# Performance work log

Hardware: AMD Instinct MI355X
Metric: run time of the kernel (lower is better)

Reference implementation:

```python
import jax, jax.numpy as jnp
import numpy as np

B, S = 2, 2048
HQ, HKV, D = 32, 8, 128
SCALING = 0.08838834764831845  # 1/sqrt(128)
E4M3_MAX = 448.0
FP4_MAX = 6.0
# e2m1 representable magnitudes and decision midpoints
FP4_GRID = jnp.array([0.0, 0.5, 1.0, 1.5, 2.0, 3.0, 4.0, 6.0], dtype=jnp.float32)
FP4_MID = (FP4_GRID[:-1] + FP4_GRID[1:]) / 2.0


def quant_dequant_e4m3(x):
    """Simulate torch .to(float8_e4m3fn): clamp to +-448, round mantissa to 3 bits."""
    ax = jnp.abs(x)
    xc = jnp.clip(x, -E4M3_MAX, E4M3_MAX)
    e = jnp.clip(jnp.floor(jnp.log2(jnp.maximum(ax, 1e-12))), -6.0, 8.0)
    q = jnp.round(xc * jnp.exp2(3.0 - e)) * jnp.exp2(e - 3.0)
    return jnp.where(ax == 0.0, 0.0, q)


def quant_dequant_fp4(x):
    """FP4 (e2m1) compress/decompress with per-(token,head) absmax scale over head_dim.
    x: [B, S, H, D] -> dequantized [B, S, H, D]."""
    scale = jnp.max(jnp.abs(x), axis=-1, keepdims=True) / FP4_MAX  # [B,S,H,1]
    scale = jnp.maximum(scale, 1e-12)
    xn = x / scale
    idx = jnp.searchsorted(FP4_MID, jnp.abs(xn))  # nearest e2m1 magnitude
    return jnp.sign(xn) * FP4_GRID[idx] * scale


def setup_inputs() -> dict:
    key = jax.random.key(0)
    kq, kk, kv = jax.random.split(key, 3)
    q = jax.random.normal(kq, (B, S, HQ * D), dtype=jnp.float32)
    k = jax.random.normal(kk, (B, S, HKV * D), dtype=jnp.float32)
    v = jax.random.normal(kv, (B, S, HKV * D), dtype=jnp.float32)
    return {"q": q, "k": k, "v": v}


def reference(q, k, v):
    # reshape to heads
    qh = q.reshape(B, S, HQ, D)
    kh = k.reshape(B, S, HKV, D)
    vh = v.reshape(B, S, HKV, D)
    # FP8 cast then FP4 compress/decompress of the KV cache
    kq8 = quant_dequant_e4m3(kh)
    vq8 = quant_dequant_e4m3(vh)
    kd = quant_dequant_fp4(kq8)
    vd = quant_dequant_fp4(vq8)
    # GQA: expand kv heads to query heads
    g = HQ // HKV
    kr = jnp.repeat(kd, g, axis=2)  # [B,S,HQ,D]
    vr = jnp.repeat(vd, g, axis=2)
    scores = jnp.einsum("bqhd,bkhd->bhqk", qh, kr) * SCALING  # [B,HQ,S,S]
    causal = jnp.tril(jnp.ones((S, S), dtype=bool))
    scores = jnp.where(causal[None, None], scores, jnp.float32(-1e30))
    probs = jax.nn.softmax(scores, axis=-1)
    out = jnp.einsum("bhqk,bkhd->bqhd", probs, vr)
    return out.reshape(B, S, HQ * D)
```

## Files before the change

### kernel.cpp

```cpp
#include <hip/hip_runtime.h>
#include <cstdint>
#include <cstddef>

#define B_    2
#define S_    2048
#define HQ_   32
#define HKV_  8
#define D_    128
#define QSCALE_ (0.08838834764831845f * 1.4426950408889634f)

#define NROW_ (B_*S_*HKV_)

typedef __bf16 bf16x8 __attribute__((ext_vector_type(8)));
typedef float  f32x4  __attribute__((ext_vector_type(4)));
typedef unsigned int u32x4 __attribute__((ext_vector_type(4)));

__device__ __forceinline__ unsigned int f2bfu(float f) {
    __bf16 b = (__bf16)f;
    return (unsigned int)__builtin_bit_cast(unsigned short, b);
}

__device__ __forceinline__ void gl_lds16(const unsigned short* g, unsigned short* l) {
    __builtin_amdgcn_global_load_lds(
        (const __attribute__((address_space(1))) void*)g,
        (__attribute__((address_space(3))) void*)l, 16, 0, 0);
}

__device__ __forceinline__ float qd_e4m3(float x) {
    float ax = fabsf(x);
    float xc = fminf(fmaxf(x, -448.f), 448.f);
    float axc = fmaxf(ax, 1e-12f);
    int e = (int)((__builtin_bit_cast(unsigned int, axc) >> 23) & 255u) - 127;
    e = min(max(e, -6), 8);
    float s1 = __builtin_bit_cast(float, (unsigned int)(130 - e) << 23);
    float s2 = __builtin_bit_cast(float, (unsigned int)(124 + e) << 23);
    float q = rintf(xc * s1) * s2;
    return ax == 0.f ? 0.f : q;
}

__device__ __forceinline__ float qd_fp4(float x, float scale) {
    float xn = x / scale;
    float a = fabsf(xn);
    float g;
    if      (a <= 0.25f) g = 0.f;
    else if (a <= 0.75f) g = 0.5f;
    else if (a <= 1.25f) g = 1.f;
    else if (a <= 1.75f) g = 1.5f;
    else if (a <= 2.5f)  g = 2.f;
    else if (a <= 3.5f)  g = 3.f;
    else if (a <= 5.f)   g = 4.f;
    else                 g = 6.f;
    return copysignf(g * scale, xn);
}

__global__ __launch_bounds__(256) void prep(const float* __restrict__ k,
                                            const float* __restrict__ v,
                                            unsigned short* __restrict__ kd,
                                            unsigned short* __restrict__ vdT) {
    __shared__ alignas(16) unsigned short t[64][136];
    if (blockIdx.x < 8192) {
        int gw = (blockIdx.x * 256 + threadIdx.x) >> 6;
        int lane = threadIdx.x & 63;
        int row = gw;
        int b   = row / (S_ * HKV_);
        int rem = row - b * (S_ * HKV_);
        int s   = rem >> 3;
        int h   = rem & 7;
        float2 x = *(const float2*)(k + (size_t)row * D_ + 2 * lane);
        float q0 = qd_e4m3(x.x);
        float q1 = qd_e4m3(x.y);
        float amax = fmaxf(fabsf(q0), fabsf(q1));
#pragma unroll
        for (int m = 1; m < 64; m <<= 1) amax = fmaxf(amax, __shfl_xor(amax, m, 64));
        float scale = fmaxf(amax / 6.0f, 1e-12f);
        float y0 = qd_fp4(q0, scale);
        float y1 = qd_fp4(q1, scale);
        size_t outOff = ((size_t)(b * HKV_ + h) * S_ + s) * D_ + 2 * lane;
        unsigned int pack = f2bfu(y0) | (f2bfu(y1) << 16);
        *(unsigned int*)(kd + outOff) = pack;
    } else {
        int bid = blockIdx.x - 8192;
        int bh = bid >> 5;
        int st = bid & 31;
        int s0 = st * 64;
        int b = bh >> 3;
        int h = bh & 7;
        int tid = threadIdx.x;
        int lane = tid & 63;
        int wave = tid >> 6;
#pragma unroll
        for (int i = 0; i < 8; ++i) {
            int rA = wave * 16 + 2 * i;
            const float* srcA = v + (((size_t)b * S_ + (s0 + rA)) * HKV_ + h) * D_ + 2 * lane;
            const float* srcB = srcA + (size_t)HKV_ * D_;
            float2 xA = *(const float2*)srcA;
            float2 xB = *(const float2*)srcB;
            float a0 = qd_e4m3(xA.x), a1 = qd_e4m3(xA.y);
            float c0 = qd_e4m3(xB.x), c1 = qd_e4m3(xB.y);
            float amA = fmaxf(fabsf(a0), fabsf(a1));
            float amB = fmaxf(fabsf(c0), fabsf(c1));
#pragma unroll
            for (int m = 1; m < 64; m <<= 1) {
                amA = fmaxf(amA, __shfl_xor(amA, m, 64));
                amB = fmaxf(amB, __shfl_xor(amB, m, 64));
            }
            float sA = fmaxf(amA / 6.0f, 1e-12f);
            float sB = fmaxf(amB / 6.0f, 1e-12f);
            unsigned int pA = f2bfu(qd_fp4(a0, sA)) | (f2bfu(qd_fp4(a1, sA)) << 16);
            unsigned int pB = f2bfu(qd_fp4(c0, sB)) | (f2bfu(qd_fp4(c1, sB)) << 16);
            *(unsigned int*)&t[rA][2 * lane]     = pA;
            *(unsigned int*)&t[rA + 1][2 * lane] = pB;
        }
        __syncthreads();
        int d = tid >> 1;
        unsigned short* dp = vdT + ((size_t)bh * D_ + d) * S_ + s0;
#pragma unroll
        for (int i = 0; i < 4; ++i) {
            int c = (tid & 1) + 2 * i;
            int so = c * 8;
            unsigned short tmp[8];
#pragma unroll
            for (int e = 0; e < 8; ++e) tmp[e] = t[so + e][d];
            *(uint4*)(dp + so) = *(uint4*)tmp;
        }
    }
}

__global__ __launch_bounds__(256) void attn(const float* __restrict__ q,
                                            const unsigned short* __restrict__ kd,
                                            const unsigned short* __restrict__ vdT,
                                            float* __restrict__ out) {
    int bh = blockIdx.x;
    int qt = 31 - blockIdx.y;
    int b  = bh >> 5;
    int hq = bh & 31;
    int hkv = hq >> 2;
    int tid  = threadIdx.x;
    int lane = tid & 63;
    int wave = tid >> 6;
    int m16  = lane & 15;
    int g    = lane >> 4;
    int m8   = m16 & 7;

    __shared__ alignas(16) unsigned short ks[64 * 128];
    __shared__ alignas(16) unsigned short vs[128 * 64];

    const unsigned short* kbase = kd  + (size_t)(b * HKV_ + hkv) * S_ * D_;
    const unsigned short* vbase = vdT + (size_t)(b * HKV_ + hkv) * D_ * S_;

    bf16x8 vones;
#pragma unroll
    for (int j = 0; j < 8; ++j) vones[j] = (__bf16)1.0f;

    int q0 = qt * 64;
    int qrowBase = q0 + wave * 16;

    bf16x8 qf[4];
    const float* qp = q + (((size_t)b * S_ + (qrowBase + m16)) * HQ_ + hq) * D_;
#pragma unroll
    for (int c = 0; c < 4; ++c) {
        const float* p0 = qp + c * 32 + g * 8;
        bf16x8 f;
#pragma unroll
        for (int j = 0; j < 8; ++j) f[j] = (__bf16)(p0[j] * QSCALE_);
        qf[c] = f;
    }

    f32x4 o[8];
#pragma unroll
    for (int i = 0; i < 8; ++i) o[i] = (f32x4){0.f, 0.f, 0.f, 0.f};
    f32x4 o9 = (f32x4){0.f, 0.f, 0.f, 0.f};

    for (int kt = 0; kt <= qt; ++kt) {
        int k0 = kt * 64;
        __syncthreads();
#pragma unroll
        for (int i = 0; i < 4; ++i) {
            int row = wave * 16 + i * 4 + (lane >> 4);
            int c = (lane & 15) ^ (row & 15);
            gl_lds16(kbase + (size_t)(k0 + row) * D_ + c * 8,
                     &ks[wave * 2048 + i * 512]);
        }
#pragma unroll
        for (int i = 0; i < 4; ++i) {
            int d = wave * 32 + i * 8 + (lane >> 3);
            int c = (lane & 7) ^ (d & 7);
            gl_lds16(vbase + (size_t)d * S_ + k0 + c * 8,
                     &vs[wave * 2048 + i * 512]);
        }
        __syncthreads();

        bool diag = (kt == qt);
        int kcmax = diag ? ((wave >> 1) + 1) : 2;

        f32x4 sacc[4];
#pragma unroll
        for (int n = 0; n < 4; ++n) sacc[n] = (f32x4){0.f, 0.f, 0.f, 0.f};
        __builtin_amdgcn_s_setprio(1);
#pragma unroll
        for (int n = 0; n < 4; ++n) {
            if (!diag || n <= wave) {
#pragma unroll
                for (int c = 0; c < 4; ++c) {
                    bf16x8 ak = *(const bf16x8*)&ks[(n * 16 + m16) * 128 +
                                                    (((c * 4 + g) ^ m16) * 8)];
                    sacc[n] = __builtin_amdgcn_mfma_f32_16x16x32_bf16(ak, qf[c], sacc[n], 0, 0, 0);
                }
            }
        }
        __builtin_amdgcn_s_setprio(0);

        int qloc = wave * 16 + m16;
        unsigned int Dlo[4], Dhi[4];
#pragma unroll
        for (int n = 0; n < 4; ++n) {
            if (!diag || n <= wave) {
                float pr[4];
#pragma unroll
                for (int r = 0; r < 4; ++r) {
                    float p = exp2f(sacc[n][r]);
                    if (diag) {
                        int key = n * 16 + g * 4 + r;
                        p = (key <= qloc) ? p : 0.f;
                    }
                    pr[r] = p;
                }
                Dlo[n] = f2bfu(pr[0]) | (f2bfu(pr[1]) << 16);
                Dhi[n] = f2bfu(pr[2]) | (f2bfu(pr[3]) << 16);
            } else {
                Dlo[n] = 0u; Dhi[n] = 0u;
            }
        }

        __builtin_amdgcn_s_setprio(1);
#pragma unroll
        for (int kc = 0; kc < 2; ++kc) {
            if (kc < kcmax) {
                auto p0 = __builtin_amdgcn_permlane32_swap(Dlo[2 * kc], Dlo[2 * kc + 1], false, false);
                auto p1 = __builtin_amdgcn_permlane32_swap(Dhi[2 * kc], Dhi[2 * kc + 1], false, false);
                auto r0 = __builtin_amdgcn_permlane16_swap(p0[0], p0[1], false, false);
                auto r1 = __builtin_amdgcn_permlane16_swap(p1[0], p1[1], false, false);
                u32x4 pau = (u32x4){r0[0], r1[0], r0[1], r1[1]};
                bf16x8 pa = __builtin_bit_cast(bf16x8, pau);
                o9 = __builtin_amdgcn_mfma_f32_16x16x32_bf16(pa, vones, o9, 0, 0, 0);
#pragma unroll
                for (int ds = 0; ds < 8; ++ds) {
                    bf16x8 vb = *(const bf16x8*)&vs[(ds * 16 + m16) * 64 +
                                                    (((kc * 4 + g) ^ m8) * 8)];
                    o[ds] = __builtin_amdgcn_mfma_f32_16x16x32_bf16(pa, vb, o[ds], 0, 0, 0);
                }
            }
        }
        __builtin_amdgcn_s_setprio(0);
    }

#pragma unroll
    for (int r = 0; r < 4; ++r) {
        float inv = 1.f / o9[r];
        float* op = out + (((size_t)b * S_ + (qrowBase + g * 4 + r)) * HQ_ + hq) * D_;
#pragma unroll
        for (int ds = 0; ds < 8; ++ds)
            op[ds * 16 + m16] = o[ds][r] * inv;
    }
}

extern "C" void kernel_launch(void* const* d_in, const int* in_sizes, int n_in,
                              void* d_out, int out_size, void* d_ws, size_t ws_size,
                              hipStream_t stream) {
    const float* q = (const float*)d_in[0];
    const float* k = (const float*)d_in[1];
    const float* v = (const float*)d_in[2];
    float* out = (float*)d_out;

    unsigned short* kd  = (unsigned short*)d_ws;
    unsigned short* vdT = kd + (size_t)NROW_ * D_;

    prep<<<8704, 256, 0, stream>>>(k, v, kd, vdT);
    attn<<<dim3(64, 32), 256, 0, stream>>>(q, kd, vdT, out);
}
```

Measured before the change: 255.4 us.

## Process 128 query rows per block with two 16-row tiles per wave

Each block now covers 128 query rows, with every wave handling two 16-row subtiles. This lets each K/V LDS tile feed twice as many MFMAs and halves the grid. The K/V load loop is also restructured to split the K and V waits with vmcnt-based partial waits and raw barriers, and launch bounds ask for 3 blocks per CU. In exchange, register pressure roughly doubles for accumulators and there are fewer blocks to balance the causal triangle.

```diff
diff --git a/kernel.cpp b/kernel.cpp
--- a/kernel.cpp
+++ b/kernel.cpp
@@ -126,12 +126,22 @@
     }
 }
 
-__global__ __launch_bounds__(256) void attn(const float* __restrict__ q,
-                                            const unsigned short* __restrict__ kd,
-                                            const unsigned short* __restrict__ vdT,
-                                            float* __restrict__ out) {
+__device__ __forceinline__ bf16x8 permpack(const unsigned int* Dlo,
+                                           const unsigned int* Dhi, int kc) {
+    auto p0 = __builtin_amdgcn_permlane32_swap(Dlo[2 * kc], Dlo[2 * kc + 1], false, false);
+    auto p1 = __builtin_amdgcn_permlane32_swap(Dhi[2 * kc], Dhi[2 * kc + 1], false, false);
+    auto r0 = __builtin_amdgcn_permlane16_swap(p0[0], p0[1], false, false);
+    auto r1 = __builtin_amdgcn_permlane16_swap(p1[0], p1[1], false, false);
+    u32x4 pau = (u32x4){r0[0], r1[0], r0[1], r1[1]};
+    return __builtin_bit_cast(bf16x8, pau);
+}
+
+__global__ __launch_bounds__(256, 3) void attn(const float* __restrict__ q,
+                                               const unsigned short* __restrict__ kd,
+                                               const unsigned short* __restrict__ vdT,
+                                               float* __restrict__ out) {
     int bh = blockIdx.x;
-    int qt = 31 - blockIdx.y;
+    int qt = 15 - blockIdx.y;
     int b  = bh >> 5;
     int hq = bh & 31;
     int hkv = hq >> 2;
@@ -152,115 +162,176 @@
 #pragma unroll
     for (int j = 0; j < 8; ++j) vones[j] = (__bf16)1.0f;
 
-    int q0 = qt * 64;
-    int qrowBase = q0 + wave * 16;
-
-    bf16x8 qf[4];
-    const float* qp = q + (((size_t)b * S_ + (qrowBase + m16)) * HQ_ + hq) * D_;
-#pragma unroll
-    for (int c = 0; c < 4; ++c) {
-        const float* p0 = qp + c * 32 + g * 8;
-        bf16x8 f;
-#pragma unroll
-        for (int j = 0; j < 8; ++j) f[j] = (__bf16)(p0[j] * QSCALE_);
-        qf[c] = f;
-    }
-
-    f32x4 o[8];
-#pragma unroll
-    for (int i = 0; i < 8; ++i) o[i] = (f32x4){0.f, 0.f, 0.f, 0.f};
-    f32x4 o9 = (f32x4){0.f, 0.f, 0.f, 0.f};
-
-    for (int kt = 0; kt <= qt; ++kt) {
-        int k0 = kt * 64;
-        __syncthreads();
+    int q0 = qt * 128;
+    int nkt = 2 * qt + 2;
+
+    auto stage = [&](int k0s) {
 #pragma unroll
         for (int i = 0; i < 4; ++i) {
             int row = wave * 16 + i * 4 + (lane >> 4);
             int c = (lane & 15) ^ (row & 15);
-            gl_lds16(kbase + (size_t)(k0 + row) * D_ + c * 8,
+            gl_lds16(kbase + (size_t)(k0s + row) * D_ + c * 8,
                      &ks[wave * 2048 + i * 512]);
         }
 #pragma unroll
         for (int i = 0; i < 4; ++i) {
             int d = wave * 32 + i * 8 + (lane >> 3);
             int c = (lane & 7) ^ (d & 7);
-            gl_lds16(vbase + (size_t)d * S_ + k0 + c * 8,
+            gl_lds16(vbase + (size_t)d * S_ + k0s + c * 8,
                      &vs[wave * 2048 + i * 512]);
         }
-        __syncthreads();
-
-        bool diag = (kt == qt);
-        int kcmax = diag ? ((wave >> 1) + 1) : 2;
-
-        f32x4 sacc[4];
-#pragma unroll
-        for (int n = 0; n < 4; ++n) sacc[n] = (f32x4){0.f, 0.f, 0.f, 0.f};
-        __builtin_amdgcn_s_setprio(1);
-#pragma unroll
-        for (int n = 0; n < 4; ++n) {
-            if (!diag || n <= wave) {
-#pragma unroll
-                for (int c = 0; c < 4; ++c) {
-                    bf16x8 ak = *(const bf16x8*)&ks[(n * 16 + m16) * 128 +
-                                                    (((c * 4 + g) ^ m16) * 8)];
-                    sacc[n] = __builtin_amdgcn_mfma_f32_16x16x32_bf16(ak, qf[c], sacc[n], 0, 0, 0);
+    };
+
+    stage(0);
+
+    bf16x8 qf0[4], qf1[4];
+    {
+        const float* qp0 = q + (((size_t)b * S_ + (q0 + wave * 32 + m16)) * HQ_ + hq) * D_;
+        const float* qp1 = qp0 + (size_t)16 * HQ_ * D_;
+#pragma unroll
+        for (int c = 0; c < 4; ++c) {
+            const float* a0 = qp0 + c * 32 + g * 8;
+            const float* a1 = qp1 + c * 32 + g * 8;
+            bf16x8 f0, f1;
+#pragma unroll
+            for (int j = 0; j < 8; ++j) {
+                f0[j] = (__bf16)(a0[j] * QSCALE_);
+                f1[j] = (__bf16)(a1[j] * QSCALE_);
+            }
+            qf0[c] = f0;
+            qf1[c] = f1;
+        }
+    }
+
+    f32x4 o0[8], o1[8];
+#pragma unroll
+    for (int i = 0; i < 8; ++i) { o0[i] = (f32x4){0.f,0.f,0.f,0.f}; o1[i] = (f32x4){0.f,0.f,0.f,0.f}; }
+    f32x4 l0 = (f32x4){0.f,0.f,0.f,0.f};
+    f32x4 l1 = (f32x4){0.f,0.f,0.f,0.f};
+
+    for (int kt = 0; kt < nkt; ++kt) {
+        int k0 = kt * 64;
+        if (kt) stage(k0);
+
+        asm volatile("s_waitcnt vmcnt(4)" ::: "memory");
+        __builtin_amdgcn_s_barrier();
+
+        int base1 = (q0 - k0) + wave * 32 + 16;
+        int base0 = base1 - 16;
+        int a1 = 0, a0 = 0, kcm1 = 0, kcm0 = 0;
+        unsigned int Dlo1[4], Dhi1[4], Dlo0[4], Dhi0[4];
+        if (base1 >= 0) {
+            bool full1 = base1 >= 64, full0 = base0 >= 64;
+            a1 = full1 ? 4 : ((base1 >> 4) + 1);
+            a0 = (base0 < 0) ? 0 : (full0 ? 4 : ((base0 >> 4) + 1));
+            kcm1 = (a1 + 1) >> 1;
+            kcm0 = (a0 + 1) >> 1;
+
+            f32x4 s0[4], s1[4];
+#pragma unroll
+            for (int n = 0; n < 4; ++n) {
+                s0[n] = (f32x4){0.f,0.f,0.f,0.f};
+                s1[n] = (f32x4){0.f,0.f,0.f,0.f};
+            }
+            __builtin_amdgcn_s_setprio(1);
+#pragma unroll
+            for (int n = 0; n < 4; ++n) {
+                if (n < a1) {
+#pragma unroll
+                    for (int c = 0; c < 4; ++c) {
+                        bf16x8 ak = *(const bf16x8*)&ks[(n * 16 + m16) * 128 +
+                                                        (((c * 4 + g) ^ m16) * 8)];
+                        s1[n] = __builtin_amdgcn_mfma_f32_16x16x32_bf16(ak, qf1[c], s1[n], 0, 0, 0);
+                        if (n < a0)
+                            s0[n] = __builtin_amdgcn_mfma_f32_16x16x32_bf16(ak, qf0[c], s0[n], 0, 0, 0);
+                    }
                 }
             }
-        }
-        __builtin_amdgcn_s_setprio(0);
-
-        int qloc = wave * 16 + m16;
-        unsigned int Dlo[4], Dhi[4];
-#pragma unroll
-        for (int n = 0; n < 4; ++n) {
-            if (!diag || n <= wave) {
-                float pr[4];
-#pragma unroll
-                for (int r = 0; r < 4; ++r) {
-                    float p = exp2f(sacc[n][r]);
-                    if (diag) {
-                        int key = n * 16 + g * 4 + r;
-                        p = (key <= qloc) ? p : 0.f;
+            __builtin_amdgcn_s_setprio(0);
+
+#pragma unroll
+            for (int n = 0; n < 4; ++n) {
+                if (n < a1) {
+                    float pr[4];
+#pragma unroll
+                    for (int r = 0; r < 4; ++r) {
+                        float p = exp2f(s1[n][r]);
+                        if (!full1) {
+                            int key = n * 16 + g * 4 + r;
+                            p = (key <= base1 + m16) ? p : 0.f;
+                        }
+                        pr[r] = p;
                     }
-                    pr[r] = p;
+                    Dlo1[n] = f2bfu(pr[0]) | (f2bfu(pr[1]) << 16);
+                    Dhi1[n] = f2bfu(pr[2]) | (f2bfu(pr[3]) << 16);
+                } else { Dlo1[n] = 0u; Dhi1[n] = 0u; }
+            }
+            if (a0 > 0) {
+#pragma unroll
+                for (int n = 0; n < 4; ++n) {
+                    if (n < a0) {
+                        float pr[4];
+#pragma unroll
+                        for (int r = 0; r < 4; ++r) {
+                            float p = exp2f(s0[n][r]);
+                            if (!full0) {
+                                int key = n * 16 + g * 4 + r;
+                                p = (key <= base0 + m16) ? p : 0.f;
+                            }
+                            pr[r] = p;
+                        }
+                        Dlo0[n] = f2bfu(pr[0]) | (f2bfu(pr[1]) << 16);
+                        Dhi0[n] = f2bfu(pr[2]) | (f2bfu(pr[3]) << 16);
+                    } else { Dlo0[n] = 0u; Dhi0[n] = 0u; }
                 }
-                Dlo[n] = f2bfu(pr[0]) | (f2bfu(pr[1]) << 16);
-                Dhi[n] = f2bfu(pr[2]) | (f2bfu(pr[3]) << 16);
-            } else {
-                Dlo[n] = 0u; Dhi[n] = 0u;
-            }
-        }
-
-        __builtin_amdgcn_s_setprio(1);
-#pragma unroll
-        for (int kc = 0; kc < 2; ++kc) {
-            if (kc < kcmax) {
-                auto p0 = __builtin_amdgcn_permlane32_swap(Dlo[2 * kc], Dlo[2 * kc + 1], false, false);
-                auto p1 = __builtin_amdgcn_permlane32_swap(Dhi[2 * kc], Dhi[2 * kc + 1], false, false);
-                auto r0 = __builtin_amdgcn_permlane16_swap(p0[0], p0[1], false, false);
-                auto r1 = __builtin_amdgcn_permlane16_swap(p1[0], p1[1], false, false);
-                u32x4 pau = (u32x4){r0[0], r1[0], r0[1], r1[1]};
-                bf16x8 pa = __builtin_bit_cast(bf16x8, pau);
-                o9 = __builtin_amdgcn_mfma_f32_16x16x32_bf16(pa, vones, o9, 0, 0, 0);
-#pragma unroll
-                for (int ds = 0; ds < 8; ++ds) {
-                    bf16x8 vb = *(const bf16x8*)&vs[(ds * 16 + m16) * 64 +
-                                                    (((kc * 4 + g) ^ m8) * 8)];
-                    o[ds] = __builtin_amdgcn_mfma_f32_16x16x32_bf16(pa, vb, o[ds], 0, 0, 0);
+            }
+        }
+
+        asm volatile("s_waitcnt vmcnt(0)" ::: "memory");
+        __builtin_amdgcn_s_barrier();
+
+        if (base1 >= 0) {
+            __builtin_amdgcn_s_setprio(1);
+#pragma unroll
+            for (int kc = 0; kc < 2; ++kc) {
+                if (kc < kcm1) {
+                    bf16x8 pa1 = permpack(Dlo1, Dhi1, kc);
+                    l1 = __builtin_amdgcn_mfma_f32_16x16x32_bf16(pa1, vones, l1, 0, 0, 0);
+                    bool use0 = kc < kcm0;
+                    bf16x8 pa0;
+                    if (use0) {
+                        pa0 = permpack(Dlo0, Dhi0, kc);
+                        l0 = __builtin_amdgcn_mfma_f32_16x16x32_bf16(pa0, vones, l0, 0, 0, 0);
+                    }
+#pragma unroll
+                    for (int ds = 0; ds < 8; ++ds) {
+                        bf16x8 vb = *(const bf16x8*)&vs[(ds * 16 + m16) * 64 +
+                                                        (((kc * 4 + g) ^ m8) * 8)];
+                        o1[ds] = __builtin_amdgcn_mfma_f32_16x16x32_bf16(pa1, vb, o1[ds], 0, 0, 0);
+                        if (use0)
+                            o0[ds] = __builtin_amdgcn_mfma_f32_16x16x32_bf16(pa0, vb, o0[ds], 0, 0, 0);
+                    }
                 }
             }
-        }
-        __builtin_amdgcn_s_setprio(0);
+            __builtin_amdgcn_s_setprio(0);
+        }
+
+        asm volatile("s_waitcnt lgkmcnt(0)" ::: "memory");
+        __builtin_amdgcn_s_barrier();
     }
 
 #pragma unroll
     for (int r = 0; r < 4; ++r) {
-        float inv = 1.f / o9[r];
-        float* op = out + (((size_t)b * S_ + (qrowBase + g * 4 + r)) * HQ_ + hq) * D_;
+        float inv0 = 1.f / l0[r];
+        float* op0 = out + (((size_t)b * S_ + (q0 + wave * 32 + g * 4 + r)) * HQ_ + hq) * D_;
 #pragma unroll
         for (int ds = 0; ds < 8; ++ds)
-            op[ds * 16 + m16] = o[ds][r] * inv;
+            op0[ds * 16 + m16] = o0[ds][r] * inv0;
+        float inv1 = 1.f / l1[r];
+        float* op1 = op0 + (size_t)16 * HQ_ * D_;
+#pragma unroll
+        for (int ds = 0; ds < 8; ++ds)
+            op1[ds * 16 + m16] = o1[ds][r] * inv1;
     }
 }
 
@@ -276,5 +347,5 @@
     unsigned short* vdT = kd + (size_t)NROW_ * D_;
 
     prep<<<8704, 256, 0, stream>>>(k, v, kd, vdT);
-    attn<<<dim3(64, 32), 256, 0, stream>>>(q, kd, vdT, out);
-}
+    attn<<<dim3(64, 16), 256, 0, stream>>>(q, kd, vdT, out);
+}
```

After: 319.3 us. 25.0% more time.

## Software-pipeline attention loop: defer PV of previous tile, double-buffer V, prefetch next tiles

Applied to the files above, without the earlier changes.

Restructures the main attention loop into a software pipeline. The QK^T of tile kt now overlaps with the PV MFMAs of tile kt-1 and with the exp2 work, while the next K tile and a double-buffered V tile are prefetched asynchronously using explicit waitcnt and barriers. The goal is to hide global-to-LDS load latency and the exp/permlane work behind MFMA execution. It costs extra LDS for the second V buffer and live registers for the deferred probability fragments, and the hand-written vmcnt waits and barriers are fragile.

```diff
diff --git a/kernel.cpp b/kernel.cpp
--- a/kernel.cpp
+++ b/kernel.cpp
@@ -126,6 +126,16 @@
     }
 }
 
+__device__ __forceinline__ bf16x8 permpack(const unsigned int* Dlo,
+                                           const unsigned int* Dhi, int kc) {
+    auto p0 = __builtin_amdgcn_permlane32_swap(Dlo[2 * kc], Dlo[2 * kc + 1], false, false);
+    auto p1 = __builtin_amdgcn_permlane32_swap(Dhi[2 * kc], Dhi[2 * kc + 1], false, false);
+    auto r0 = __builtin_amdgcn_permlane16_swap(p0[0], p0[1], false, false);
+    auto r1 = __builtin_amdgcn_permlane16_swap(p1[0], p1[1], false, false);
+    u32x4 pau = (u32x4){r0[0], r1[0], r0[1], r1[1]};
+    return __builtin_bit_cast(bf16x8, pau);
+}
+
 __global__ __launch_bounds__(256) void attn(const float* __restrict__ q,
                                             const unsigned short* __restrict__ kd,
                                             const unsigned short* __restrict__ vdT,
@@ -143,7 +153,7 @@
     int m8   = m16 & 7;
 
     __shared__ alignas(16) unsigned short ks[64 * 128];
-    __shared__ alignas(16) unsigned short vs[128 * 64];
+    __shared__ alignas(16) unsigned short vs[2][128 * 64];
 
     const unsigned short* kbase = kd  + (size_t)(b * HKV_ + hkv) * S_ * D_;
     const unsigned short* vbase = vdT + (size_t)(b * HKV_ + hkv) * D_ * S_;
@@ -152,8 +162,30 @@
 #pragma unroll
     for (int j = 0; j < 8; ++j) vones[j] = (__bf16)1.0f;
 
+    auto stageK = [&](int k0s) {
+#pragma unroll
+        for (int i = 0; i < 4; ++i) {
+            int row = wave * 16 + i * 4 + (lane >> 4);
+            int c = (lane & 15) ^ (row & 15);
+            gl_lds16(kbase + (size_t)(k0s + row) * D_ + c * 8,
+                     &ks[wave * 2048 + i * 512]);
+        }
+    };
+    auto stageV = [&](int buf, int k0s) {
+#pragma unroll
+        for (int i = 0; i < 4; ++i) {
+            int d = wave * 32 + i * 8 + (lane >> 3);
+            int c = (lane & 7) ^ (d & 7);
+            gl_lds16(vbase + (size_t)d * S_ + k0s + c * 8,
+                     &vs[buf][wave * 2048 + i * 512]);
+        }
+    };
+
     int q0 = qt * 64;
     int qrowBase = q0 + wave * 16;
+
+    stageK(0);
+    stageV(0, 0);
 
     bf16x8 qf[4];
     const float* qp = q + (((size_t)b * S_ + (qrowBase + m16)) * HQ_ + hq) * D_;
@@ -170,28 +202,15 @@
 #pragma unroll
     for (int i = 0; i < 8; ++i) o[i] = (f32x4){0.f, 0.f, 0.f, 0.f};
     f32x4 o9 = (f32x4){0.f, 0.f, 0.f, 0.f};
+    bf16x8 paPrev0, paPrev1;
+
+    int qloc = wave * 16 + m16;
 
     for (int kt = 0; kt <= qt; ++kt) {
-        int k0 = kt * 64;
-        __syncthreads();
-#pragma unroll
-        for (int i = 0; i < 4; ++i) {
-            int row = wave * 16 + i * 4 + (lane >> 4);
-            int c = (lane & 15) ^ (row & 15);
-            gl_lds16(kbase + (size_t)(k0 + row) * D_ + c * 8,
-                     &ks[wave * 2048 + i * 512]);
-        }
-#pragma unroll
-        for (int i = 0; i < 4; ++i) {
-            int d = wave * 32 + i * 8 + (lane >> 3);
-            int c = (lane & 7) ^ (d & 7);
-            gl_lds16(vbase + (size_t)d * S_ + k0 + c * 8,
-                     &vs[wave * 2048 + i * 512]);
-        }
-        __syncthreads();
+        asm volatile("s_waitcnt vmcnt(4)" ::: "memory");
+        __builtin_amdgcn_s_barrier();
 
         bool diag = (kt == qt);
-        int kcmax = diag ? ((wave >> 1) + 1) : 2;
 
         f32x4 sacc[4];
 #pragma unroll
@@ -210,10 +229,13 @@
         }
         __builtin_amdgcn_s_setprio(0);
 
-        int qloc = wave * 16 + m16;
+        asm volatile("s_waitcnt lgkmcnt(0)" ::: "memory");
+        __builtin_amdgcn_s_barrier();
+        if (kt < qt) stageK((kt + 1) * 64);
+
         unsigned int Dlo[4], Dhi[4];
 #pragma unroll
-        for (int n = 0; n < 4; ++n) {
+        for (int n = 0; n < 2; ++n) {
             if (!diag || n <= wave) {
                 float pr[4];
 #pragma unroll
@@ -227,31 +249,73 @@
                 }
                 Dlo[n] = f2bfu(pr[0]) | (f2bfu(pr[1]) << 16);
                 Dhi[n] = f2bfu(pr[2]) | (f2bfu(pr[3]) << 16);
-            } else {
-                Dlo[n] = 0u; Dhi[n] = 0u;
-            }
-        }
-
-        __builtin_amdgcn_s_setprio(1);
-#pragma unroll
-        for (int kc = 0; kc < 2; ++kc) {
-            if (kc < kcmax) {
-                auto p0 = __builtin_amdgcn_permlane32_swap(Dlo[2 * kc], Dlo[2 * kc + 1], false, false);
-                auto p1 = __builtin_amdgcn_permlane32_swap(Dhi[2 * kc], Dhi[2 * kc + 1], false, false);
-                auto r0 = __builtin_amdgcn_permlane16_swap(p0[0], p0[1], false, false);
-                auto r1 = __builtin_amdgcn_permlane16_swap(p1[0], p1[1], false, false);
-                u32x4 pau = (u32x4){r0[0], r1[0], r0[1], r1[1]};
-                bf16x8 pa = __builtin_bit_cast(bf16x8, pau);
-                o9 = __builtin_amdgcn_mfma_f32_16x16x32_bf16(pa, vones, o9, 0, 0, 0);
-#pragma unroll
-                for (int ds = 0; ds < 8; ++ds) {
-                    bf16x8 vb = *(const bf16x8*)&vs[(ds * 16 + m16) * 64 +
-                                                    (((kc * 4 + g) ^ m8) * 8)];
-                    o[ds] = __builtin_amdgcn_mfma_f32_16x16x32_bf16(pa, vb, o[ds], 0, 0, 0);
+            } else { Dlo[n] = 0u; Dhi[n] = 0u; }
+        }
+        bf16x8 paNew0 = permpack(Dlo, Dhi, 0);
+        if (kt > 0) {
+            int pb = (kt - 1) & 1;
+            o9 = __builtin_amdgcn_mfma_f32_16x16x32_bf16(paPrev0, vones, o9, 0, 0, 0);
+#pragma unroll
+            for (int ds = 0; ds < 8; ++ds) {
+                bf16x8 vb = *(const bf16x8*)&vs[pb][(ds * 16 + m16) * 64 + ((g ^ m8) * 8)];
+                o[ds] = __builtin_amdgcn_mfma_f32_16x16x32_bf16(paPrev0, vb, o[ds], 0, 0, 0);
+            }
+        }
+#pragma unroll
+        for (int n = 2; n < 4; ++n) {
+            if (!diag || n <= wave) {
+                float pr[4];
+#pragma unroll
+                for (int r = 0; r < 4; ++r) {
+                    float p = exp2f(sacc[n][r]);
+                    if (diag) {
+                        int key = n * 16 + g * 4 + r;
+                        p = (key <= qloc) ? p : 0.f;
+                    }
+                    pr[r] = p;
                 }
-            }
-        }
-        __builtin_amdgcn_s_setprio(0);
+                Dlo[n] = f2bfu(pr[0]) | (f2bfu(pr[1]) << 16);
+                Dhi[n] = f2bfu(pr[2]) | (f2bfu(pr[3]) << 16);
+            } else { Dlo[n] = 0u; Dhi[n] = 0u; }
+        }
+        bf16x8 paNew1 = permpack(Dlo, Dhi, 1);
+        if (kt > 0) {
+            int pb = (kt - 1) & 1;
+            o9 = __builtin_amdgcn_mfma_f32_16x16x32_bf16(paPrev1, vones, o9, 0, 0, 0);
+#pragma unroll
+            for (int ds = 0; ds < 8; ++ds) {
+                bf16x8 vb = *(const bf16x8*)&vs[pb][(ds * 16 + m16) * 64 + (((4 + g) ^ m8) * 8)];
+                o[ds] = __builtin_amdgcn_mfma_f32_16x16x32_bf16(paPrev1, vb, o[ds], 0, 0, 0);
+            }
+        }
+
+        asm volatile("s_waitcnt lgkmcnt(0)" ::: "memory");
+        __builtin_amdgcn_s_barrier();
+        if (kt < qt) stageV((kt + 1) & 1, (kt + 1) * 64);
+
+        paPrev0 = paNew0;
+        paPrev1 = paNew1;
+    }
+
+    asm volatile("s_waitcnt vmcnt(0)" ::: "memory");
+    __builtin_amdgcn_s_barrier();
+    {
+        int pb = qt & 1;
+        int kcmax = (wave >> 1) + 1;
+        o9 = __builtin_amdgcn_mfma_f32_16x16x32_bf16(paPrev0, vones, o9, 0, 0, 0);
+#pragma unroll
+        for (int ds = 0; ds < 8; ++ds) {
+            bf16x8 vb = *(const bf16x8*)&vs[pb][(ds * 16 + m16) * 64 + ((g ^ m8) * 8)];
+            o[ds] = __builtin_amdgcn_mfma_f32_16x16x32_bf16(paPrev0, vb, o[ds], 0, 0, 0);
+        }
+        if (kcmax > 1) {
+            o9 = __builtin_amdgcn_mfma_f32_16x16x32_bf16(paPrev1, vones, o9, 0, 0, 0);
+#pragma unroll
+            for (int ds = 0; ds < 8; ++ds) {
+                bf16x8 vb = *(const bf16x8*)&vs[pb][(ds * 16 + m16) * 64 + (((4 + g) ^ m8) * 8)];
+                o[ds] = __builtin_amdgcn_mfma_f32_16x16x32_bf16(paPrev1, vb, o[ds], 0, 0, 0);
+            }
+        }
     }
 
 #pragma unroll
```

After: 250.4 us. -2.0%, faster.
